# Optimization experiments

Hardware: AMD Instinct MI355X
Metric: run time of the kernel (lower is better)

## Reference

```python
import jax, jax.numpy as jnp
import numpy as np

BS, FH, FW, NA = 32, 100, 100, 9
IMG_H, IMG_W = 1600, 1600
STRIDE = 16
KEEP_PRE, KEEP_POST, NMS_THR = 1000, 300, 0.7


def _grid_anchors():
    scales = np.array([128.0, 256.0, 512.0])
    ratios = np.array([0.5, 1.0, 2.0])
    ws, hs = [], []
    for s in scales:
        for r in ratios:
            ws.append(s * np.sqrt(1.0 / r))
            hs.append(s * np.sqrt(r))
    ws, hs = np.array(ws), np.array(hs)  # [9]
    sx = (np.arange(FW) + 0.5) * STRIDE
    sy = (np.arange(FH) + 0.5) * STRIDE
    cx, cy = np.meshgrid(sx, sy)  # [FH,FW]
    cx = cx.reshape(-1, 1)
    cy = cy.reshape(-1, 1)
    anchors = np.stack([
        cx - 0.5 * ws, cy - 0.5 * hs, cx + 0.5 * ws, cy + 0.5 * hs
    ], axis=-1).reshape(-1, 4)  # [FH*FW*NA, 4]
    return anchors.astype(np.float32)


def setup_inputs() -> dict:
    key = jax.random.key(0)
    k1, k2 = jax.random.split(key)
    N = FH * FW * NA
    cls_logits = jax.random.normal(k1, (BS, N, 1), dtype=jnp.float32)
    reg_deltas = jax.random.normal(k2, (BS, N, 4), dtype=jnp.float32) * 0.3
    anchors = jnp.asarray(_grid_anchors())
    return {"cls_logits": cls_logits, "reg_deltas": reg_deltas,
            "anchors": anchors, "img_h": IMG_H, "img_w": IMG_W}


def _offsets2boxes(deltas, anchors):
    # deltas: [bs,N,4] (dx,dy,dw,dh); anchors: [N,4] xyxy
    aw = anchors[:, 2] - anchors[:, 0]
    ah = anchors[:, 3] - anchors[:, 1]
    acx = anchors[:, 0] + 0.5 * aw
    acy = anchors[:, 1] + 0.5 * ah
    cx = deltas[..., 0] * aw + acx
    cy = deltas[..., 1] * ah + acy
    w = jnp.exp(deltas[..., 2]) * aw
    h = jnp.exp(deltas[..., 3]) * ah
    return jnp.stack([cx - 0.5 * w, cy - 0.5 * h, cx + 0.5 * w, cy + 0.5 * h], axis=-1)


def _iou_matrix(b):
    # b: [K,4] -> [K,K]
    area = (b[:, 2] - b[:, 0]) * (b[:, 3] - b[:, 1])
    lt = jnp.maximum(b[:, None, :2], b[None, :, :2])
    rb = jnp.minimum(b[:, None, 2:], b[None, :, 2:])
    wh = jnp.clip(rb - lt, 0.0)
    inter = wh[..., 0] * wh[..., 1]
    return inter / (area[:, None] + area[None, :] - inter + 1e-12)


def _detect_single(boxes, scores, img_h, img_w):
    # boxes: [N,4], scores: [N]
    top_scores, idx = jax.lax.top_k(scores, KEEP_PRE)
    b = boxes[idx]  # [K,4], already score-sorted descending
    b = jnp.stack([
        jnp.clip(b[:, 0], 0.0, img_w), jnp.clip(b[:, 1], 0.0, img_h),
        jnp.clip(b[:, 2], 0.0, img_w), jnp.clip(b[:, 3], 0.0, img_h)
    ], axis=-1)
    iou = _iou_matrix(b)  # [K,K]
    K = KEEP_PRE
    cols = jnp.arange(K)

    def body(i, keep):
        # if box i still kept, suppress later boxes with IoU > thr (greedy NMS)
        sup = keep[i] & (iou[i] > NMS_THR) & (cols > i)
        return keep & ~sup

    keep = jax.lax.fori_loop(0, K, body, jnp.ones((K,), dtype=bool))
    # kept boxes first (stable sort preserves descending-score order), take top P
    order = jnp.argsort(~keep, stable=True)[:KEEP_POST]
    valid = keep[order]
    det = jnp.concatenate([b[order], top_scores[order, None]], axis=-1)
    return det * valid[:, None].astype(det.dtype)  # padded rows zeroed


def reference(cls_logits, reg_deltas, anchors, img_h, img_w):
    bs = cls_logits.shape[0]
    scores = jax.nn.sigmoid(cls_logits.reshape(bs, -1))  # [bs,N]
    boxes = _offsets2boxes(reg_deltas.reshape(bs, -1, 4), anchors)  # [bs,N,4]
    fh = jnp.float32(img_h)
    fw = jnp.float32(img_w)
    dets = jax.vmap(lambda b, s: _detect_single(b, s, fh, fw))(boxes, scores)
    return dets  # [bs, KEEP_POST, 5] (xmin,ymin,xmax,ymax,score), zero-padded
```

## Files before the change

### kernel.cpp

```cpp
#include <hip/hip_runtime.h>
#include <stdint.h>

#pragma clang fp contract(off)

#define BS 32
#define NANCH 90000
#define KEEP_PRE 1000
#define KEEP_POST 300
#define NMS_THR 0.7f
#define NBINS 4096
#define CAND_MAX 4096
#define MW 16
#define CNT_STRIDE 32
#define NSLICE 8

typedef unsigned long long u64;
typedef unsigned int u32;

#define HIST_BYTES ((size_t)BS * NBINS * 4)
#define CNT_OFF    (HIST_BYTES)
#define CNT_BYTES  ((size_t)BS * CNT_STRIDE * 4)
#define BTHR_OFF   (CNT_OFF + CNT_BYTES)
#define CAND_OFF   (BTHR_OFF + 128)
#define BOX_OFF    (CAND_OFF + (size_t)BS * CAND_MAX * 8)
#define SCORE_OFF  (BOX_OFF + (size_t)BS * KEEP_PRE * 16)
#define MASK_OFF   (SCORE_OFF + (size_t)BS * KEEP_PRE * 4)

__device__ __forceinline__ u32 fmono(float f) {
    u32 u = __float_as_uint(f);
    return (u & 0x80000000u) ? ~u : (u | 0x80000000u);
}

__global__ __launch_bounds__(256) void hist_kernel(const float* __restrict__ logits,
                                                   u32* __restrict__ hist) {
    __shared__ u32 lh[NBINS];
    const int b = blockIdx.y;
    for (int i = threadIdx.x; i < NBINS; i += 256) lh[i] = 0;
    __syncthreads();
    const float* src = logits + (size_t)b * NANCH;
    const int stride = 256 * gridDim.x;
    for (int i = blockIdx.x * 256 + threadIdx.x; i < NANCH; i += stride) {
        u32 m = fmono(src[i]);
        atomicAdd(&lh[m >> 20], 1u);
    }
    __syncthreads();
    u32* gh = hist + (size_t)b * NBINS;
    for (int i = threadIdx.x; i < NBINS; i += 256)
        if (lh[i]) atomicAdd(&gh[i], lh[i]);
}

__global__ __launch_bounds__(256) void thresh_kernel(const u32* __restrict__ hist,
                                                     u32* __restrict__ Bthr) {
    __shared__ u32 part[256];
    const int b = blockIdx.x;
    const u32* h = hist + (size_t)b * NBINS;
    u32 s = 0;
    for (int k = 0; k < 16; k++) s += h[threadIdx.x * 16 + k];
    part[threadIdx.x] = s;
    __syncthreads();
    if (threadIdx.x == 0) {
        u32 cum = 0;
        int c = 255;
        for (; c >= 0; c--) {
            if (cum + part[c] >= KEEP_PRE) break;
            cum += part[c];
        }
        if (c < 0) c = 0;
        int bin = c * 16 + 15;
        for (; bin >= c * 16; bin--) {
            if (cum + h[bin] >= KEEP_PRE) break;
            cum += h[bin];
        }
        if (bin < c * 16) bin = c * 16;
        Bthr[b] = (u32)bin;
    }
}

__global__ __launch_bounds__(256) void compact_kernel(const float* __restrict__ logits,
                                                      const u32* __restrict__ Bthr,
                                                      u32* __restrict__ cnt,
                                                      u64* __restrict__ cand) {
    const int b = blockIdx.y;
    const int i = blockIdx.x * 256 + threadIdx.x;
    __shared__ u32 blk_cnt;
    __shared__ u32 blk_base;
    if (threadIdx.x == 0) blk_cnt = 0;
    __syncthreads();
    bool is_cand = false;
    u32 m = 0;
    if (i < NANCH) {
        m = fmono(logits[(size_t)b * NANCH + i]);
        is_cand = (m >> 20) >= Bthr[b];
    }
    u64 ballot = __ballot(is_cand);
    const u32 lane = threadIdx.x & 63;
    u32 wbase = 0;
    u32 old = 0;
    if (ballot) {
        if (lane == 0) old = atomicAdd(&blk_cnt, (u32)__popcll(ballot));
        wbase = __shfl(old, 0);
    }
    __syncthreads();
    if (threadIdx.x == 0 && blk_cnt)
        blk_base = atomicAdd(&cnt[b * CNT_STRIDE], blk_cnt);
    __syncthreads();
    if (is_cand) {
        u32 prefix = (u32)__popcll(ballot & ((1ull << lane) - 1ull));
        u32 pos = blk_base + wbase + prefix;
        if (pos < CAND_MAX)
            cand[(size_t)b * CAND_MAX + pos] = ((u64)m << 32) | (u32)(~(u32)i);
    }
}

__global__ __launch_bounds__(256) void select_kernel(const float* __restrict__ deltas,
                                                     const float* __restrict__ anchors,
                                                     const u32* __restrict__ cnt,
                                                     const u64* __restrict__ cand,
                                                     float4* __restrict__ selbox,
                                                     float* __restrict__ selscore,
                                                     const int* __restrict__ p_img_h,
                                                     const int* __restrict__ p_img_w) {
    __shared__ u64 keys[CAND_MAX];
    const int b = blockIdx.y;
    const int slice = blockIdx.x;
    const int n = (int)min(cnt[b * CNT_STRIDE], (u32)CAND_MAX);
    const u64* src = cand + (size_t)b * CAND_MAX;
    for (int i = threadIdx.x; i < n; i += 256)
        keys[i] = src[i];
    __syncthreads();
    const int per = (n + NSLICE - 1) / NSLICE;
    const int i0 = slice * per;
    const int i1 = min(i0 + per, n);
    const float W = (float)(*p_img_w);
    const float H = (float)(*p_img_h);
    const float4* d4 = (const float4*)deltas;
    const float4* a4 = (const float4*)anchors;
    for (int i = i0 + threadIdx.x; i < i1; i += 256) {
        const u64 me = keys[i];
        int rank = 0;
        int j = 0;
        for (; j + 16 <= n; j += 16) {
            int r0 = 0;
#pragma unroll
            for (int k = 0; k < 16; k++) r0 += (keys[j + k] > me);
            rank += r0;
        }
        for (; j < n; j++) rank += (keys[j] > me);
        if (rank < KEEP_PRE) {
            u32 idx = ~(u32)me;
            u32 m = (u32)(me >> 32);
            u32 ub = (m & 0x80000000u) ? (m ^ 0x80000000u) : ~m;
            float logit = __uint_as_float(ub);
            float score = 1.0f / (1.0f + expf(-logit));
            float4 d = d4[(size_t)b * NANCH + idx];
            float4 a = a4[idx];
            float aw = a.z - a.x, ah = a.w - a.y;
            float acx = a.x + 0.5f * aw, acy = a.y + 0.5f * ah;
            float cx = d.x * aw + acx, cy = d.y * ah + acy;
            float w = expf(d.z) * aw, h = expf(d.w) * ah;
            float x1 = cx - 0.5f * w, y1 = cy - 0.5f * h;
            float x2 = cx + 0.5f * w, y2 = cy + 0.5f * h;
            x1 = fminf(fmaxf(x1, 0.0f), W); y1 = fminf(fmaxf(y1, 0.0f), H);
            x2 = fminf(fmaxf(x2, 0.0f), W); y2 = fminf(fmaxf(y2, 0.0f), H);
            selbox[(size_t)b * KEEP_PRE + rank] = make_float4(x1, y1, x2, y2);
            selscore[(size_t)b * KEEP_PRE + rank] = score;
        }
    }
}

__global__ __launch_bounds__(256) void iou_kernel(const float4* __restrict__ selbox,
                                                  u64* __restrict__ mask) {
    const int b = blockIdx.y;
    const int w = blockIdx.x & 15;
    const int chunk = blockIdx.x >> 4;
    const int i = chunk * 256 + threadIdx.x;
    __shared__ float4 cb[64];
    __shared__ float ca[64];
    if (threadIdx.x < 64) {
        int j = w * 64 + threadIdx.x;
        float4 bx = (j < KEEP_PRE) ? selbox[(size_t)b * KEEP_PRE + j]
                                   : make_float4(0, 0, 0, 0);
        cb[threadIdx.x] = bx;
        ca[threadIdx.x] = (bx.z - bx.x) * (bx.w - bx.y);
    }
    __syncthreads();
    if (i >= KEEP_PRE) return;
    float4 bi = selbox[(size_t)b * KEEP_PRE + i];
    float ai = (bi.z - bi.x) * (bi.w - bi.y);
    u64 bits = 0;
    const int jbase = w * 64;
    for (int jj = 0; jj < 64; jj++) {
        int j = jbase + jj;
        if (j > i && j < KEEP_PRE) {
            float4 bj = cb[jj];
            float ltx = fmaxf(bi.x, bj.x), lty = fmaxf(bi.y, bj.y);
            float rbx = fminf(bi.z, bj.z), rby = fminf(bi.w, bj.w);
            float wx = fmaxf(rbx - ltx, 0.0f), wy = fmaxf(rby - lty, 0.0f);
            float inter = wx * wy;
            float denom = ai + ca[jj] - inter + 1e-12f;
            if (inter / denom > NMS_THR) bits |= (1ull << jj);
        }
    }
    mask[((size_t)b * KEEP_PRE + i) * MW + w] = bits;
}

#define CH_ROWS 64
#define CH_WORDS (CH_ROWS * MW)
#define NCHUNK ((KEEP_PRE + CH_ROWS - 1) / CH_ROWS)

__global__ __launch_bounds__(256) void nms_out_kernel(const u64* __restrict__ mask,
                                                      const float4* __restrict__ selbox,
                                                      const float* __restrict__ selscore,
                                                      float* __restrict__ out) {
    const int b = blockIdx.x;
    __shared__ u64 lbuf[2][CH_WORDS];
    __shared__ u64 keepw[MW];
    __shared__ u32 wpre[MW + 1];
    __shared__ int ls_stop;
    const int tid = threadIdx.x;
    const u64* mrow = mask + (size_t)b * KEEP_PRE * MW;

    auto load_chunk = [&](int c) {
        int idx = tid - 128;
        if (idx < 0) return;
        const int words = (c == NCHUNK - 1)
                            ? (KEEP_PRE - (NCHUNK - 1) * CH_ROWS) * MW
                            : CH_WORDS;
        const u64* gsrc = mrow + (size_t)c * CH_WORDS;
        u64* dst = lbuf[c & 1];
#pragma unroll
        for (int k = 0; k < 4; k++) {
            int off = k * 256 + idx * 2;
            ulonglong2 v;
            if (off < words) v = *(const ulonglong2*)(gsrc + off);
            else { v.x = 0ull; v.y = 0ull; }
            *(ulonglong2*)(dst + off) = v;
        }
    };

    if (tid == 0) ls_stop = 0;
    load_chunk(0);
    __syncthreads();

    u64 remv = 0;
    int kept_total = 0;
    const int lw = tid & 15;
    for (int c = 0; c < NCHUNK; c++) {
        if (c + 1 < NCHUNK) load_chunk(c + 1);
        if (tid < 64) {
            const u64* lb = lbuf[c & 1];
            u64 cur = __shfl(remv, c);
#pragma unroll
            for (int blk = 0; blk < 8; blk++) {
                u64 R[8], rwv[8];
#pragma unroll
                for (int k = 0; k < 8; k++)
                    R[k] = lb[(size_t)(blk * 8 + k) * MW + lw];
#pragma unroll
                for (int k = 0; k < 8; k++)
                    rwv[k] = lb[(size_t)(blk * 8 + k) * MW + c];
#pragma unroll
                for (int k = 0; k < 8; k++) {
                    const int p = blk * 8 + k;
                    u64 msk = ((cur >> p) & 1ull) ? 0ull : ~0ull;
                    remv |= R[k] & msk;
                    cur  |= rwv[k] & msk;
                }
            }
            kept_total += 64 - (int)__popcll(cur);
            if (c + 1 < NCHUNK && kept_total >= KEEP_POST) {
                if (lw > c) remv = ~0ull;
                if (tid == 0) ls_stop = 1;
            }
        }
        __syncthreads();
        if (ls_stop) break;
    }

    if (tid < MW) {
        u64 kw = ~remv;
        if (tid == MW - 1) kw &= (1ull << (KEEP_PRE - 64 * (MW - 1))) - 1ull;
        keepw[tid] = kw;
    }
    __syncthreads();
    if (tid == 0) {
        u32 cnt = 0;
        for (int w = 0; w < MW; w++) { wpre[w] = cnt; cnt += (u32)__popcll(keepw[w]); }
        wpre[MW] = cnt;
    }
    __syncthreads();
    const int total = (int)wpre[MW];
    float* outb = out + (size_t)b * KEEP_POST * 5;
    for (int i = tid; i < KEEP_PRE; i += 256) {
        int w = i >> 6;
        u64 kw = keepw[w];
        if ((kw >> (i & 63)) & 1ull) {
            int rank = (int)wpre[w] + __popcll(kw & ((1ull << (i & 63)) - 1ull));
            if (rank < KEEP_POST) {
                float4 bx = selbox[(size_t)b * KEEP_PRE + i];
                float sc = selscore[(size_t)b * KEEP_PRE + i];
                outb[rank * 5 + 0] = bx.x;
                outb[rank * 5 + 1] = bx.y;
                outb[rank * 5 + 2] = bx.z;
                outb[rank * 5 + 3] = bx.w;
                outb[rank * 5 + 4] = sc;
            }
        }
    }
    for (int r = tid; r < KEEP_POST; r += 256) {
        if (r >= total) {
            outb[r * 5 + 0] = 0.0f;
            outb[r * 5 + 1] = 0.0f;
            outb[r * 5 + 2] = 0.0f;
            outb[r * 5 + 3] = 0.0f;
            outb[r * 5 + 4] = 0.0f;
        }
    }
}

extern "C" void kernel_launch(void* const* d_in, const int* in_sizes, int n_in,
                              void* d_out, int out_size, void* d_ws, size_t ws_size,
                              hipStream_t stream) {
    const float* logits  = (const float*)d_in[0];
    const float* deltas  = (const float*)d_in[1];
    const float* anchors = (const float*)d_in[2];
    const int* p_img_h   = (const int*)d_in[3];
    const int* p_img_w   = (const int*)d_in[4];

    char* ws = (char*)d_ws;
    u32* hist     = (u32*)(ws);
    u32* cnt      = (u32*)(ws + CNT_OFF);
    u32* Bthr     = (u32*)(ws + BTHR_OFF);
    u64* cand     = (u64*)(ws + CAND_OFF);
    float4* selbox = (float4*)(ws + BOX_OFF);
    float* selscore = (float*)(ws + SCORE_OFF);
    u64* mask     = (u64*)(ws + MASK_OFF);

    hipMemsetAsync(ws, 0, CNT_OFF + CNT_BYTES, stream);

    hist_kernel<<<dim3(16, BS), 256, 0, stream>>>(logits, hist);
    thresh_kernel<<<BS, 256, 0, stream>>>(hist, Bthr);
    compact_kernel<<<dim3((NANCH + 255) / 256, BS), 256, 0, stream>>>(logits, Bthr, cnt, cand);
    select_kernel<<<dim3(NSLICE, BS), 256, 0, stream>>>(deltas, anchors, cnt, cand,
                                                        selbox, selscore, p_img_h, p_img_w);
    iou_kernel<<<dim3(64, BS), 256, 0, stream>>>(selbox, mask);
    nms_out_kernel<<<BS, 256, 0, stream>>>(mask, selbox, selscore, (float*)d_out);
}
```

Measured before the change: 187.3 us.

## Fuse histogram, threshold and compaction into one per-batch kernel; trim IoU blocks

Replaces the memset plus the histogram, threshold and compaction kernels with a single 1024-thread block per image. That block builds a duplicated shared histogram from float4 loads, finds the threshold bin with a wave scan, and compacts candidates with a shared-memory counter. The IoU kernel now launches only the upper-triangular tiles (40 instead of 64 blocks per image) and applies the triangle and bounds masks after a branch-free unrolled loop. NMS masks out stale lower words before they are read. The fusion removes launches and global atomics, but with only 32 blocks the scan of the logits runs on a small part of the GPU.

Result: faster. 178.0 us (-4.9%).

```diff
diff --git a/kernel.cpp b/kernel.cpp
--- a/kernel.cpp
+++ b/kernel.cpp
@@ -9,19 +9,19 @@
 #define KEEP_POST 300
 #define NMS_THR 0.7f
 #define NBINS 4096
+#define HREP 4129
 #define CAND_MAX 4096
 #define MW 16
 #define CNT_STRIDE 32
 #define NSLICE 8
+#define NF4 22500
 
 typedef unsigned long long u64;
 typedef unsigned int u32;
 
-#define HIST_BYTES ((size_t)BS * NBINS * 4)
-#define CNT_OFF    (HIST_BYTES)
+#define CNT_OFF    0
 #define CNT_BYTES  ((size_t)BS * CNT_STRIDE * 4)
-#define BTHR_OFF   (CNT_OFF + CNT_BYTES)
-#define CAND_OFF   (BTHR_OFF + 128)
+#define CAND_OFF   (CNT_OFF + CNT_BYTES)
 #define BOX_OFF    (CAND_OFF + (size_t)BS * CAND_MAX * 8)
 #define SCORE_OFF  (BOX_OFF + (size_t)BS * KEEP_PRE * 16)
 #define MASK_OFF   (SCORE_OFF + (size_t)BS * KEEP_PRE * 4)
@@ -31,85 +31,108 @@
     return (u & 0x80000000u) ? ~u : (u | 0x80000000u);
 }
 
-__global__ __launch_bounds__(256) void hist_kernel(const float* __restrict__ logits,
-                                                   u32* __restrict__ hist) {
-    __shared__ u32 lh[NBINS];
-    const int b = blockIdx.y;
-    for (int i = threadIdx.x; i < NBINS; i += 256) lh[i] = 0;
-    __syncthreads();
-    const float* src = logits + (size_t)b * NANCH;
-    const int stride = 256 * gridDim.x;
-    for (int i = blockIdx.x * 256 + threadIdx.x; i < NANCH; i += stride) {
-        u32 m = fmono(src[i]);
-        atomicAdd(&lh[m >> 20], 1u);
-    }
-    __syncthreads();
-    u32* gh = hist + (size_t)b * NBINS;
-    for (int i = threadIdx.x; i < NBINS; i += 256)
-        if (lh[i]) atomicAdd(&gh[i], lh[i]);
-}
-
-__global__ __launch_bounds__(256) void thresh_kernel(const u32* __restrict__ hist,
-                                                     u32* __restrict__ Bthr) {
-    __shared__ u32 part[256];
+__global__ __launch_bounds__(1024) void prep_kernel(const float* __restrict__ logits,
+                                                    u32* __restrict__ cnt,
+                                                    u64* __restrict__ cand) {
+    __shared__ u32 lh[2][HREP];
+    __shared__ u32 parts[1024];
+    __shared__ u32 s_B;
+    __shared__ u32 s_cnt;
     const int b = blockIdx.x;
-    const u32* h = hist + (size_t)b * NBINS;
-    u32 s = 0;
-    for (int k = 0; k < 16; k++) s += h[threadIdx.x * 16 + k];
-    part[threadIdx.x] = s;
-    __syncthreads();
-    if (threadIdx.x == 0) {
-        u32 cum = 0;
-        int c = 255;
-        for (; c >= 0; c--) {
-            if (cum + part[c] >= KEEP_PRE) break;
-            cum += part[c];
-        }
-        if (c < 0) c = 0;
-        int bin = c * 16 + 15;
-        for (; bin >= c * 16; bin--) {
-            if (cum + h[bin] >= KEEP_PRE) break;
-            cum += h[bin];
-        }
-        if (bin < c * 16) bin = c * 16;
-        Bthr[b] = (u32)bin;
-    }
-}
-
-__global__ __launch_bounds__(256) void compact_kernel(const float* __restrict__ logits,
-                                                      const u32* __restrict__ Bthr,
-                                                      u32* __restrict__ cnt,
-                                                      u64* __restrict__ cand) {
-    const int b = blockIdx.y;
-    const int i = blockIdx.x * 256 + threadIdx.x;
-    __shared__ u32 blk_cnt;
-    __shared__ u32 blk_base;
-    if (threadIdx.x == 0) blk_cnt = 0;
-    __syncthreads();
-    bool is_cand = false;
-    u32 m = 0;
-    if (i < NANCH) {
-        m = fmono(logits[(size_t)b * NANCH + i]);
-        is_cand = (m >> 20) >= Bthr[b];
-    }
-    u64 ballot = __ballot(is_cand);
-    const u32 lane = threadIdx.x & 63;
-    u32 wbase = 0;
-    u32 old = 0;
-    if (ballot) {
-        if (lane == 0) old = atomicAdd(&blk_cnt, (u32)__popcll(ballot));
-        wbase = __shfl(old, 0);
-    }
-    __syncthreads();
-    if (threadIdx.x == 0 && blk_cnt)
-        blk_base = atomicAdd(&cnt[b * CNT_STRIDE], blk_cnt);
-    __syncthreads();
-    if (is_cand) {
-        u32 prefix = (u32)__popcll(ballot & ((1ull << lane) - 1ull));
-        u32 pos = blk_base + wbase + prefix;
-        if (pos < CAND_MAX)
-            cand[(size_t)b * CAND_MAX + pos] = ((u64)m << 32) | (u32)(~(u32)i);
-    }
+    const int tid = threadIdx.x;
+    u32* h0 = lh[0];
+    u32* h1 = lh[1];
+
+    for (int i = tid; i < 2 * HREP; i += 1024) ((u32*)lh)[i] = 0;
+    if (tid == 0) s_cnt = 0;
+    __syncthreads();
+
+    const float4* src4 = (const float4*)(logits + (size_t)b * NANCH);
+    u32* myh = lh[tid & 1];
+
+#define H1_(f) do { u32 m_ = fmono(f); atomicAdd(&myh[m_ >> 20], 1u); } while (0)
+#define HIST4_(v) do { H1_((v).x); H1_((v).y); H1_((v).z); H1_((v).w); } while (0)
+
+    for (int j = 0; j < 20; j += 4) {
+        float4 va = src4[tid + (j + 0) * 1024];
+        float4 vb = src4[tid + (j + 1) * 1024];
+        float4 vc = src4[tid + (j + 2) * 1024];
+        float4 vd = src4[tid + (j + 3) * 1024];
+        HIST4_(va); HIST4_(vb); HIST4_(vc); HIST4_(vd);
+    }
+    {
+        float4 ve = src4[tid + 20 * 1024];
+        HIST4_(ve);
+        if (tid < NF4 - 21 * 1024) {
+            float4 vf = src4[tid + 21 * 1024];
+            HIST4_(vf);
+        }
+    }
+    __syncthreads();
+
+    {
+        int g = tid * 4;
+        parts[tid] = h0[g] + h1[g] + h0[g + 1] + h1[g + 1]
+                   + h0[g + 2] + h1[g + 2] + h0[g + 3] + h1[g + 3];
+    }
+    __syncthreads();
+    if (tid < 64) {
+        u32 g64 = 0;
+#pragma unroll
+        for (int k = 0; k < 16; k++) g64 += parts[tid * 16 + k];
+        u32 s = g64;
+#pragma unroll
+        for (int off = 1; off < 64; off <<= 1) {
+            u32 x = __shfl_down(s, off);
+            if (tid + off < 64) s += x;
+        }
+        if (s >= KEEP_PRE && (s - g64) < KEEP_PRE) {
+            u32 cum = s - g64;
+            int stop = tid * 64;
+            int bin = stop + 63;
+            u32 B = (u32)stop;
+            for (; bin >= stop; bin--) {
+                u32 hb = h0[bin] + h1[bin];
+                if (cum + hb >= KEEP_PRE) { B = (u32)bin; break; }
+                cum += hb;
+            }
+            s_B = B;
+        }
+    }
+    __syncthreads();
+    const u32 B = s_B;
+
+    const u32 lane = tid & 63;
+    u64* dst = cand + (size_t)b * CAND_MAX;
+    for (int j = 0; j < 22; ++j) {
+        int idx4 = tid + (j << 10);
+        bool inb = idx4 < NF4;
+        float4 v = make_float4(0.f, 0.f, 0.f, 0.f);
+        if (inb) v = src4[idx4];
+        u32 mm[4];
+        mm[0] = fmono(v.x); mm[1] = fmono(v.y); mm[2] = fmono(v.z); mm[3] = fmono(v.w);
+#pragma unroll
+        for (int k = 0; k < 4; k++) {
+            bool is = inb && ((mm[k] >> 20) >= B);
+            u64 bal = __ballot(is);
+            if (bal) {
+                u32 old = 0;
+                if (lane == 0) old = atomicAdd(&s_cnt, (u32)__popcll(bal));
+                u32 wbase = __shfl(old, 0);
+                if (is) {
+                    u32 prefix = (u32)__popcll(bal & ((1ull << lane) - 1ull));
+                    u32 pos = wbase + prefix;
+                    u32 i = (u32)(idx4 * 4 + k);
+                    if (pos < CAND_MAX)
+                        dst[pos] = ((u64)mm[k] << 32) | (u32)(~i);
+                }
+            }
+        }
+    }
+    __syncthreads();
+    if (tid == 0) cnt[b * CNT_STRIDE] = s_cnt;
+#undef H1_
+#undef HIST4_
 }
 
 __global__ __launch_bounds__(256) void select_kernel(const float* __restrict__ deltas,
@@ -171,37 +194,43 @@
 __global__ __launch_bounds__(256) void iou_kernel(const float4* __restrict__ selbox,
                                                   u64* __restrict__ mask) {
     const int b = blockIdx.y;
-    const int w = blockIdx.x & 15;
-    const int chunk = blockIdx.x >> 4;
-    const int i = chunk * 256 + threadIdx.x;
+    const int bx = blockIdx.x;
+    int c, w;
+    if (bx < 16)      { c = 0; w = bx; }
+    else if (bx < 28) { c = 1; w = bx - 12; }
+    else if (bx < 36) { c = 2; w = bx - 20; }
+    else              { c = 3; w = bx - 24; }
+    const int i = c * 256 + threadIdx.x;
     __shared__ float4 cb[64];
     __shared__ float ca[64];
     if (threadIdx.x < 64) {
         int j = w * 64 + threadIdx.x;
-        float4 bx = (j < KEEP_PRE) ? selbox[(size_t)b * KEEP_PRE + j]
-                                   : make_float4(0, 0, 0, 0);
-        cb[threadIdx.x] = bx;
-        ca[threadIdx.x] = (bx.z - bx.x) * (bx.w - bx.y);
+        float4 bx4 = (j < KEEP_PRE) ? selbox[(size_t)b * KEEP_PRE + j]
+                                    : make_float4(0, 0, 0, 0);
+        cb[threadIdx.x] = bx4;
+        ca[threadIdx.x] = (bx4.z - bx4.x) * (bx4.w - bx4.y);
     }
     __syncthreads();
     if (i >= KEEP_PRE) return;
     float4 bi = selbox[(size_t)b * KEEP_PRE + i];
     float ai = (bi.z - bi.x) * (bi.w - bi.y);
+    const int jbase = w * 64;
     u64 bits = 0;
-    const int jbase = w * 64;
+#pragma unroll 8
     for (int jj = 0; jj < 64; jj++) {
-        int j = jbase + jj;
-        if (j > i && j < KEEP_PRE) {
-            float4 bj = cb[jj];
-            float ltx = fmaxf(bi.x, bj.x), lty = fmaxf(bi.y, bj.y);
-            float rbx = fminf(bi.z, bj.z), rby = fminf(bi.w, bj.w);
-            float wx = fmaxf(rbx - ltx, 0.0f), wy = fmaxf(rby - lty, 0.0f);
-            float inter = wx * wy;
-            float denom = ai + ca[jj] - inter + 1e-12f;
-            if (inter / denom > NMS_THR) bits |= (1ull << jj);
-        }
-    }
-    mask[((size_t)b * KEEP_PRE + i) * MW + w] = bits;
+        float4 bj = cb[jj];
+        float ltx = fmaxf(bi.x, bj.x), lty = fmaxf(bi.y, bj.y);
+        float rbx = fminf(bi.z, bj.z), rby = fminf(bi.w, bj.w);
+        float wx = fmaxf(rbx - ltx, 0.0f), wy = fmaxf(rby - lty, 0.0f);
+        float inter = wx * wy;
+        float denom = ai + ca[jj] - inter + 1e-12f;
+        if (inter / denom > NMS_THR) bits |= (1ull << jj);
+    }
+    int lo = i + 1 - jbase;
+    u64 mlo = (lo <= 0) ? ~0ull : ((lo >= 64) ? 0ull : (~0ull << lo));
+    int hi = KEEP_PRE - jbase;
+    u64 mhi = (hi >= 64) ? ~0ull : ((1ull << hi) - 1ull);
+    mask[((size_t)b * KEEP_PRE + i) * MW + w] = bits & mlo & mhi;
 }
 
 #define CH_ROWS 64
@@ -249,13 +278,15 @@
         if (c + 1 < NCHUNK) load_chunk(c + 1);
         if (tid < 64) {
             const u64* lb = lbuf[c & 1];
+            const int wmin = (c >> 2) << 2;
+            const u64 vmask = (lw >= wmin) ? ~0ull : 0ull;
             u64 cur = __shfl(remv, c);
 #pragma unroll
             for (int blk = 0; blk < 8; blk++) {
                 u64 R[8], rwv[8];
 #pragma unroll
                 for (int k = 0; k < 8; k++)
-                    R[k] = lb[(size_t)(blk * 8 + k) * MW + lw];
+                    R[k] = lb[(size_t)(blk * 8 + k) * MW + lw] & vmask;
 #pragma unroll
                 for (int k = 0; k < 8; k++)
                     rwv[k] = lb[(size_t)(blk * 8 + k) * MW + c];
@@ -328,21 +359,15 @@
     const int* p_img_w   = (const int*)d_in[4];
 
     char* ws = (char*)d_ws;
-    u32* hist     = (u32*)(ws);
-    u32* cnt      = (u32*)(ws + CNT_OFF);
-    u32* Bthr     = (u32*)(ws + BTHR_OFF);
-    u64* cand     = (u64*)(ws + CAND_OFF);
+    u32* cnt       = (u32*)(ws + CNT_OFF);
+    u64* cand      = (u64*)(ws + CAND_OFF);
     float4* selbox = (float4*)(ws + BOX_OFF);
     float* selscore = (float*)(ws + SCORE_OFF);
-    u64* mask     = (u64*)(ws + MASK_OFF);
-
-    hipMemsetAsync(ws, 0, CNT_OFF + CNT_BYTES, stream);
-
-    hist_kernel<<<dim3(16, BS), 256, 0, stream>>>(logits, hist);
-    thresh_kernel<<<BS, 256, 0, stream>>>(hist, Bthr);
-    compact_kernel<<<dim3((NANCH + 255) / 256, BS), 256, 0, stream>>>(logits, Bthr, cnt, cand);
+    u64* mask      = (u64*)(ws + MASK_OFF);
+
+    prep_kernel<<<dim3(BS), 1024, 0, stream>>>(logits, cnt, cand);
     select_kernel<<<dim3(NSLICE, BS), 256, 0, stream>>>(deltas, anchors, cnt, cand,
                                                         selbox, selscore, p_img_h, p_img_w);
-    iou_kernel<<<dim3(64, BS), 256, 0, stream>>>(selbox, mask);
+    iou_kernel<<<dim3(40, BS), 256, 0, stream>>>(selbox, mask);
     nms_out_kernel<<<BS, 256, 0, stream>>>(mask, selbox, selscore, (float*)d_out);
 }
```
